# Kernel tuning notes

Measured on AMD Instinct MI355X. Metric: run time of the kernel, lower is better.

The kernel has to match this reference:

```python
import jax, jax.numpy as jnp
import numpy as np

B, D, H, E, TOPK = 65536, 1024, 512, 8, 2
LN_EPS = 1e-5
LB_WEIGHT = 0.01


def setup_inputs() -> dict:
    key = jax.random.key(0)
    ks = jax.random.split(key, 5)
    x = jax.random.normal(ks[0], (B, D), dtype=jnp.float32)
    W1 = jax.random.normal(ks[1], (D, H), dtype=jnp.float32) * 0.02
    b1 = jnp.zeros((H,), dtype=jnp.float32)
    ln_w = jnp.ones((H,), dtype=jnp.float32)
    ln_b = jnp.zeros((H,), dtype=jnp.float32)
    W2 = jax.random.normal(ks[2], (H, E), dtype=jnp.float32) * 0.02
    b2 = jnp.zeros((E,), dtype=jnp.float32)
    return {"x": x, "W1": W1, "b1": b1, "ln_w": ln_w, "ln_b": ln_b, "W2": W2, "b2": b2}


def _gate_logits(x, W1, b1, ln_w, ln_b, W2, b2):
    h = x @ W1 + b1                     # [B, H]
    mu = jnp.mean(h, axis=-1, keepdims=True)
    var = jnp.mean(jnp.square(h - mu), axis=-1, keepdims=True)
    h = (h - mu) * jax.lax.rsqrt(var + LN_EPS) * ln_w + ln_b
    h = jax.nn.gelu(h, approximate=False)  # torch nn.GELU default = exact erf
    return h @ W2 + b2                  # [B, E]


def reference(x, W1, b1, ln_w, ln_b, W2, b2):
    logits = _gate_logits(x, W1, b1, ln_w, ln_b, W2, b2)
    # sparse top-K routing (eval mode: no exploration noise)
    vals, idx = jax.lax.top_k(logits, TOPK)           # [B, K]
    rows = jnp.arange(logits.shape[0])[:, None]
    sparse = jnp.full_like(logits, -jnp.inf).at[rows, idx].set(vals)
    weights = jax.nn.softmax(sparse, axis=-1)         # zeros off top-k
    # Switch-style load-balance loss
    f = (weights > 0).astype(weights.dtype).mean(axis=0)  # fraction routed per expert
    P = weights.mean(axis=0)                              # mean gate prob per expert
    lb_loss = LB_WEIGHT * (E * jnp.sum(f * P))
    return weights, lb_loss
```

## Files before the change

### kernel.cpp

```cpp
#include <hip/hip_runtime.h>
#include <cstdint>
#include <cstddef>


typedef _Float16 f16;
typedef _Float16 f16x8 __attribute__((ext_vector_type(8)));
typedef float f32x4 __attribute__((ext_vector_type(4)));

#define B_ROWS 65536
#define D_DIM 1024
#define H_DIM 512
#define E_DIM 8
#define BM 64
#define BK 32
#define THREADS 256
#define NCHUNK 32
#define LDPX 40
#define SLABH 2560
#define BUFH 5120
#define IMG_CH (H_DIM * BK)
#define IMG_TOTAL (32 * IMG_CH)
#define GACC_OFF ((size_t)2 * IMG_TOTAL * sizeof(f16))

__global__ void prep_split(const float* __restrict__ W1,
                           f16* __restrict__ wh, f16* __restrict__ wl) {
  int id = blockIdx.x * 256 + threadIdx.x;
  int h = id & (H_DIM - 1);
  int kg = id >> 9;
  int c = kg >> 2;
  int kk0 = (kg & 3) * 8;
  int k0 = kg * 8;
  f16x8 hv, lv;
#pragma unroll
  for (int j = 0; j < 8; ++j) {
    float v = W1[(size_t)(k0 + j) * H_DIM + h] * 64.0f;
    f16 hi = (f16)v;
    hv[j] = hi;
    lv[j] = (f16)((v - (float)hi) * 256.0f);
  }
  size_t o = (size_t)c * IMG_CH + (size_t)h * BK + kk0;
  *(f16x8*)&wh[o] = hv;
  *(f16x8*)&wl[o] = lv;
}

__global__ void zero_acc(float* __restrict__ acc) {
  if (threadIdx.x < 16) acc[threadIdx.x] = 0.0f;
}

__global__ __launch_bounds__(THREADS, 2) void fused_main(
    const float* __restrict__ x,
    const f16* __restrict__ wh, const f16* __restrict__ wl,
    const float* __restrict__ b1, const float* __restrict__ lnw,
    const float* __restrict__ lnb, const float* __restrict__ W2,
    const float* __restrict__ b2, float* __restrict__ out,
    float* __restrict__ gacc) {
  __shared__ __align__(16) char pool[35584];
  f16* sx = (f16*)pool;

  const int tid = threadIdx.x;
  const int lane = tid & 63;
  const int wv = tid >> 6;
  const int l15 = lane & 15;
  const int l4 = lane >> 4;
  const int64_t row0 = (int64_t)blockIdx.x * BM;

  const int srow = tid >> 2;
  const int koff = (tid & 3) * 8;
  const int swo = srow * LDPX + koff;
  const float* xbase = x + (row0 + srow) * D_DIM + koff;

  const f16* whp = wh + (wv * 128 + l15) * BK + l4 * 8;

  f32x4 acc[4][8];
#pragma unroll
  for (int m = 0; m < 4; ++m)
#pragma unroll
    for (int n = 0; n < 8; ++n) acc[m][n] = (f32x4){0.f, 0.f, 0.f, 0.f};

  f16x8 setB[2][8];

#define ISSUE(si, C, half)                                                    \
  do {                                                                        \
    const f16* p = whp + (size_t)((C) & 31) * IMG_CH + (half) * 2048;         \
    setB[si][0] = *(const f16x8*)(p);                                         \
    setB[si][1] = *(const f16x8*)(p + 512);                                   \
    setB[si][2] = *(const f16x8*)(p + 1024);                                  \
    setB[si][3] = *(const f16x8*)(p + 1536);                                  \
    setB[si][4] = *(const f16x8*)(p + IMG_TOTAL);                             \
    setB[si][5] = *(const f16x8*)(p + IMG_TOTAL + 512);                       \
    setB[si][6] = *(const f16x8*)(p + IMG_TOTAL + 1024);                      \
    setB[si][7] = *(const f16x8*)(p + IMG_TOTAL + 1536);                      \
  } while (0)

#define CHM(MM, bufv)                                                         \
  do {                                                                        \
    const int ao = (bufv)*BUFH + ((MM)*16 + l15) * LDPX + l4 * 8;             \
    f16x8 ah = *(const f16x8*)&sx[ao];                                        \
    f16x8 al = *(const f16x8*)&sx[ao + SLABH];                                \
    f16x8 ahs;                                                                \
    _Pragma("unroll") for (int q = 0; q < 8; ++q) ahs[q] =                    \
        ah[q] * (f16)0.00390625f;                                             \
    _Pragma("unroll") for (int n = 0; n < 4; ++n)                             \
      acc[MM][n] = __builtin_amdgcn_mfma_f32_16x16x32_f16(                    \
          ah, setB[0][n], acc[MM][n], 0, 0, 0);                               \
    _Pragma("unroll") for (int n = 0; n < 4; ++n)                             \
      acc[MM][4 + n] = __builtin_amdgcn_mfma_f32_16x16x32_f16(                \
          ah, setB[1][n], acc[MM][4 + n], 0, 0, 0);                           \
    _Pragma("unroll") for (int n = 0; n < 4; ++n)                             \
      acc[MM][n] = __builtin_amdgcn_mfma_f32_16x16x32_f16(                    \
          al, setB[0][n], acc[MM][n], 0, 0, 0);                               \
    _Pragma("unroll") for (int n = 0; n < 4; ++n)                             \
      acc[MM][4 + n] = __builtin_amdgcn_mfma_f32_16x16x32_f16(                \
          al, setB[1][n], acc[MM][4 + n], 0, 0, 0);                           \
    _Pragma("unroll") for (int n = 0; n < 4; ++n)                             \
      acc[MM][n] = __builtin_amdgcn_mfma_f32_16x16x32_f16(                    \
          ahs, setB[0][4 + n], acc[MM][n], 0, 0, 0);                          \
    _Pragma("unroll") for (int n = 0; n < 4; ++n)                             \
      acc[MM][4 + n] = __builtin_amdgcn_mfma_f32_16x16x32_f16(                \
          ahs, setB[1][4 + n], acc[MM][4 + n], 0, 0, 0);                      \
  } while (0)

#define WRITE_SLAB(bufv)                                                      \
  do {                                                                        \
    float vv[8] = {xv0.x, xv0.y, xv0.z, xv0.w, xv1.x, xv1.y, xv1.z, xv1.w};   \
    f16x8 hv, lv;                                                             \
    _Pragma("unroll") for (int q = 0; q < 8; ++q) {                           \
      float t = vv[q] * 64.0f;                                                \
      f16 hh = (f16)t;                                                        \
      hv[q] = hh;                                                             \
      lv[q] = (f16)(t - (float)hh);                                           \
    }                                                                         \
    *(f16x8*)&sx[(bufv)*BUFH + swo] = hv;                                     \
    *(f16x8*)&sx[(bufv)*BUFH + SLABH + swo] = lv;                             \
  } while (0)

#define SLAB_BARRIER()                                                        \
  do {                                                                        \
    asm volatile("s_waitcnt lgkmcnt(0)" ::: "memory");                        \
    __builtin_amdgcn_s_barrier();                                             \
    __builtin_amdgcn_sched_barrier(0);                                        \
  } while (0)

  float4 xv0 = *(const float4*)(xbase);
  float4 xv1 = *(const float4*)(xbase + 4);
  WRITE_SLAB(0);
  ISSUE(0, 0, 0);
  ISSUE(1, 0, 1);
  xv0 = *(const float4*)(xbase + 32);
  xv1 = *(const float4*)(xbase + 36);
  SLAB_BARRIER();

  for (int c = 0; c < NCHUNK; ++c) {
    const int buf = c & 1;
    __builtin_amdgcn_s_setprio(1);
    CHM(0, buf);
    CHM(1, buf);
    CHM(2, buf);
    {
      const int ao = buf * BUFH + (3 * 16 + l15) * LDPX + l4 * 8;
      f16x8 ah = *(const f16x8*)&sx[ao];
      f16x8 al = *(const f16x8*)&sx[ao + SLABH];
      f16x8 ahs;
#pragma unroll
      for (int q = 0; q < 8; ++q) ahs[q] = ah[q] * (f16)0.00390625f;
#pragma unroll
      for (int n = 0; n < 4; ++n)
        acc[3][n] = __builtin_amdgcn_mfma_f32_16x16x32_f16(ah, setB[0][n], acc[3][n], 0, 0, 0);
#pragma unroll
      for (int n = 0; n < 4; ++n)
        acc[3][n] = __builtin_amdgcn_mfma_f32_16x16x32_f16(al, setB[0][n], acc[3][n], 0, 0, 0);
#pragma unroll
      for (int n = 0; n < 4; ++n)
        acc[3][n] = __builtin_amdgcn_mfma_f32_16x16x32_f16(ahs, setB[0][4 + n], acc[3][n], 0, 0, 0);
      __builtin_amdgcn_s_setprio(0);
      ISSUE(0, c + 1, 0);
      __builtin_amdgcn_s_setprio(1);
#pragma unroll
      for (int n = 0; n < 4; ++n)
        acc[3][4 + n] = __builtin_amdgcn_mfma_f32_16x16x32_f16(ah, setB[1][n], acc[3][4 + n], 0, 0, 0);
#pragma unroll
      for (int n = 0; n < 4; ++n)
        acc[3][4 + n] = __builtin_amdgcn_mfma_f32_16x16x32_f16(al, setB[1][n], acc[3][4 + n], 0, 0, 0);
#pragma unroll
      for (int n = 0; n < 4; ++n)
        acc[3][4 + n] = __builtin_amdgcn_mfma_f32_16x16x32_f16(ahs, setB[1][4 + n], acc[3][4 + n], 0, 0, 0);
      __builtin_amdgcn_s_setprio(0);
      ISSUE(1, c + 1, 1);
    }
    WRITE_SLAB(buf ^ 1);
    xv0 = *(const float4*)(xbase + ((c + 2) & 31) * 32);
    xv1 = *(const float4*)(xbase + ((c + 2) & 31) * 32 + 4);
    SLAB_BARRIER();
  }
#undef ISSUE
#undef CHM
#undef WRITE_SLAB
#undef SLAB_BARRIER
  __syncthreads();

  float* eW2T = (float*)pool;
  float* eStat = (float*)(pool + 24576);
  float* eLog = (float*)(pool + 26624);
  float* eMu = (float*)(pool + 34816);
  float* eRs = (float*)(pool + 35072);
  float* eFP = (float*)(pool + 35328);

  for (int i = tid; i < H_DIM; i += THREADS) {
    float4 wa = *(const float4*)&W2[i * 8];
    float4 wb = *(const float4*)&W2[i * 8 + 4];
    *(float4*)&eW2T[i * 12] = wa;
    *(float4*)&eW2T[i * 12 + 4] = wb;
  }
  if (tid < 16) eFP[tid] = 0.0f;

  float bb[8], lw[8], lb[8];
#pragma unroll
  for (int n = 0; n < 8; ++n) {
    int col = wv * 128 + n * 16 + l15;
    bb[n] = b1[col] * 4096.0f;
    lw[n] = lnw[col];
    lb[n] = lnb[col];
#pragma unroll
    for (int m = 0; m < 4; ++m)
#pragma unroll
      for (int r = 0; r < 4; ++r) acc[m][n][r] += bb[n];
  }

#pragma unroll
  for (int m = 0; m < 4; ++m) {
    float s1[4] = {0, 0, 0, 0};
    float s2[4] = {0, 0, 0, 0};
#pragma unroll
    for (int n = 0; n < 8; ++n)
#pragma unroll
      for (int r = 0; r < 4; ++r) {
        float vv = acc[m][n][r];
        s1[r] += vv;
        s2[r] = fmaf(vv, vv, s2[r]);
      }
#pragma unroll
    for (int d = 1; d < 16; d <<= 1)
#pragma unroll
      for (int r = 0; r < 4; ++r) {
        s1[r] += __shfl_xor(s1[r], d);
        s2[r] += __shfl_xor(s2[r], d);
      }
    if (l15 == 0) {
      int rb = m * 16 + l4 * 4;
#pragma unroll
      for (int r = 0; r < 4; ++r) {
        eStat[(wv * 64 + rb + r) * 2 + 0] = s1[r];
        eStat[(wv * 64 + rb + r) * 2 + 1] = s2[r];
      }
    }
  }
  __syncthreads();
  if (tid < BM) {
    float s1 = 0.0f, s2 = 0.0f;
#pragma unroll
    for (int w = 0; w < 4; ++w) {
      s1 += eStat[(w * 64 + tid) * 2 + 0];
      s2 += eStat[(w * 64 + tid) * 2 + 1];
    }
    float mu = s1 * (1.0f / 512.0f);
    float var = s2 * (1.0f / 512.0f) - mu * mu;
    eMu[tid] = mu;
    eRs[tid] = 1.0f / sqrtf(var + (1e-5f * 4096.0f * 4096.0f));
  }
  __syncthreads();

#pragma unroll
  for (int m = 0; m < 4; ++m) {
    int rb = m * 16 + l4 * 4;
#pragma unroll
    for (int r = 0; r < 4; ++r) {
      float mu_r = eMu[rb + r];
      float rs_r = eRs[rb + r];
      float lg[8];
#pragma unroll
      for (int e = 0; e < 8; ++e) lg[e] = 0.0f;
#pragma unroll
      for (int n = 0; n < 8; ++n) {
        int col = wv * 128 + n * 16 + l15;
        float hn = (acc[m][n][r] - mu_r) * rs_r;
        float y = fmaf(hn, lw[n], lb[n]);
        float g = 0.5f * y * (1.0f + erff(y * 0.70710678118654752440f));
        float4 w0 = *(const float4*)&eW2T[col * 12];
        float4 w1 = *(const float4*)&eW2T[col * 12 + 4];
        lg[0] = fmaf(g, w0.x, lg[0]);
        lg[1] = fmaf(g, w0.y, lg[1]);
        lg[2] = fmaf(g, w0.z, lg[2]);
        lg[3] = fmaf(g, w0.w, lg[3]);
        lg[4] = fmaf(g, w1.x, lg[4]);
        lg[5] = fmaf(g, w1.y, lg[5]);
        lg[6] = fmaf(g, w1.z, lg[6]);
        lg[7] = fmaf(g, w1.w, lg[7]);
      }
#pragma unroll
      for (int d = 1; d < 16; d <<= 1)
#pragma unroll
        for (int e = 0; e < 8; ++e) lg[e] += __shfl_xor(lg[e], d);
      if (l15 == 0) {
#pragma unroll
        for (int e = 0; e < 8; ++e) eLog[(wv * 64 + rb + r) * 8 + e] = lg[e];
      }
    }
  }
  __syncthreads();

  if (tid < BM) {
    float v[8];
#pragma unroll
    for (int e = 0; e < 8; ++e) {
      float s = b2[e];
#pragma unroll
      for (int w = 0; w < 4; ++w) s += eLog[(w * 64 + tid) * 8 + e];
      v[e] = s;
    }
    float m1 = v[0];
    int i1 = 0;
#pragma unroll
    for (int e = 1; e < 8; ++e)
      if (v[e] > m1) { m1 = v[e]; i1 = e; }
    float m2 = -3.0e38f;
    int i2 = -1;
#pragma unroll
    for (int e = 0; e < 8; ++e)
      if (e != i1 && v[e] > m2) { m2 = v[e]; i2 = e; }
    float dd = expf(m2 - m1);
    float inv = 1.0f / (1.0f + dd);
    float wA = inv, wB = dd * inv;
    float o[8];
#pragma unroll
    for (int e = 0; e < 8; ++e)
      o[e] = (e == i1) ? wA : ((e == i2) ? wB : 0.0f);
    float4* op = (float4*)&out[(row0 + tid) * 8];
    op[0] = (float4){o[0], o[1], o[2], o[3]};
    op[1] = (float4){o[4], o[5], o[6], o[7]};
    atomicAdd(&eFP[i1], 1.0f);
    atomicAdd(&eFP[i2], 1.0f);
    atomicAdd(&eFP[8 + i1], wA);
    atomicAdd(&eFP[8 + i2], wB);
  }
  __syncthreads();
  if (tid < 16) atomicAdd(&gacc[tid], eFP[tid]);
}

__global__ void lb_final(const float* __restrict__ gacc, float* __restrict__ out) {
  if (threadIdx.x == 0) {
    const float invB = 1.0f / 65536.0f;
    float s = 0.0f;
#pragma unroll
    for (int e = 0; e < 8; ++e) s += (gacc[e] * invB) * (gacc[8 + e] * invB);
    out[(size_t)B_ROWS * E_DIM] = 0.01f * 8.0f * s;
  }
}

extern "C" void kernel_launch(void* const* d_in, const int* in_sizes, int n_in,
                              void* d_out, int out_size, void* d_ws, size_t ws_size,
                              hipStream_t stream) {
  (void)in_sizes; (void)n_in; (void)out_size; (void)ws_size;
  const float* x = (const float*)d_in[0];
  const float* W1 = (const float*)d_in[1];
  const float* b1 = (const float*)d_in[2];
  const float* lnw = (const float*)d_in[3];
  const float* lnb = (const float*)d_in[4];
  const float* W2 = (const float*)d_in[5];
  const float* b2 = (const float*)d_in[6];
  float* out = (float*)d_out;
  f16* wh = (f16*)d_ws;
  f16* wl = wh + IMG_TOTAL;
  float* gacc = (float*)((char*)d_ws + GACC_OFF);

  zero_acc<<<1, 64, 0, stream>>>(gacc);
  prep_split<<<(D_DIM * H_DIM / 8) / 256, 256, 0, stream>>>(W1, wh, wl);
  fused_main<<<B_ROWS / BM, THREADS, 0, stream>>>(x, wh, wl, b1, lnw, lnb, W2, b2,
                                                  out, gacc);
  lb_final<<<1, 64, 0, stream>>>(gacc, out);
}
```

Baseline: 240.6 us.

## Double block row tile to 128 rows with 512 threads sharing W1 fragments

Each block now handles 128 rows with 8 waves arranged as 2 row groups × 4 column groups. Each W1 column slice is fetched by two waves, one per row group, so the same tile of W1 is applied to twice as many x rows and the per-row W1 load traffic is halved. In exchange the block uses more shared memory (about 46KB) and twice as many threads, which may reduce resident blocks per CU, and launch_bounds(…,2) with 512 threads may limit the registers available for the large accumulator array.

Result: slower. 251.5 us (+4.5%).

```diff
diff --git a/kernel.cpp b/kernel.cpp
--- a/kernel.cpp
+++ b/kernel.cpp
@@ -11,13 +11,13 @@
 #define D_DIM 1024
 #define H_DIM 512
 #define E_DIM 8
-#define BM 64
+#define BM 128
 #define BK 32
-#define THREADS 256
+#define THREADS 512
 #define NCHUNK 32
 #define LDPX 40
-#define SLABH 2560
-#define BUFH 5120
+#define SLABH 5120
+#define BUFH 10240
 #define IMG_CH (H_DIM * BK)
 #define IMG_TOTAL (32 * IMG_CH)
 #define GACC_OFF ((size_t)2 * IMG_TOTAL * sizeof(f16))
@@ -54,12 +54,14 @@
     const float* __restrict__ lnb, const float* __restrict__ W2,
     const float* __restrict__ b2, float* __restrict__ out,
     float* __restrict__ gacc) {
-  __shared__ __align__(16) char pool[35584];
+  __shared__ __align__(16) char pool[46208];
   f16* sx = (f16*)pool;
 
   const int tid = threadIdx.x;
   const int lane = tid & 63;
   const int wv = tid >> 6;
+  const int ng = wv & 3;
+  const int mg = wv >> 2;
   const int l15 = lane & 15;
   const int l4 = lane >> 4;
   const int64_t row0 = (int64_t)blockIdx.x * BM;
@@ -69,7 +71,7 @@
   const int swo = srow * LDPX + koff;
   const float* xbase = x + (row0 + srow) * D_DIM + koff;
 
-  const f16* whp = wh + (wv * 128 + l15) * BK + l4 * 8;
+  const f16* whp = wh + (ng * 128 + l15) * BK + l4 * 8;
 
   f32x4 acc[4][8];
 #pragma unroll
@@ -94,7 +96,7 @@
 
 #define CHM(MM, bufv)                                                         \
   do {                                                                        \
-    const int ao = (bufv)*BUFH + ((MM)*16 + l15) * LDPX + l4 * 8;             \
+    const int ao = (bufv)*BUFH + ((mg * 64 + (MM)*16 + l15)) * LDPX + l4 * 8; \
     f16x8 ah = *(const f16x8*)&sx[ao];                                        \
     f16x8 al = *(const f16x8*)&sx[ao + SLABH];                                \
     f16x8 ahs;                                                                \
@@ -157,7 +159,7 @@
     CHM(1, buf);
     CHM(2, buf);
     {
-      const int ao = buf * BUFH + (3 * 16 + l15) * LDPX + l4 * 8;
+      const int ao = buf * BUFH + (mg * 64 + 3 * 16 + l15) * LDPX + l4 * 8;
       f16x8 ah = *(const f16x8*)&sx[ao];
       f16x8 al = *(const f16x8*)&sx[ao + SLABH];
       f16x8 ahs;
@@ -200,23 +202,23 @@
 
   float* eW2T = (float*)pool;
   float* eStat = (float*)(pool + 24576);
-  float* eLog = (float*)(pool + 26624);
-  float* eMu = (float*)(pool + 34816);
-  float* eRs = (float*)(pool + 35072);
-  float* eFP = (float*)(pool + 35328);
-
-  for (int i = tid; i < H_DIM; i += THREADS) {
-    float4 wa = *(const float4*)&W2[i * 8];
-    float4 wb = *(const float4*)&W2[i * 8 + 4];
-    *(float4*)&eW2T[i * 12] = wa;
-    *(float4*)&eW2T[i * 12 + 4] = wb;
+  float* eLog = (float*)(pool + 28672);
+  float* eMu = (float*)(pool + 45056);
+  float* eRs = (float*)(pool + 45568);
+  float* eFP = (float*)(pool + 46080);
+
+  {
+    float4 wa = *(const float4*)&W2[tid * 8];
+    float4 wb = *(const float4*)&W2[tid * 8 + 4];
+    *(float4*)&eW2T[tid * 12] = wa;
+    *(float4*)&eW2T[tid * 12 + 4] = wb;
   }
   if (tid < 16) eFP[tid] = 0.0f;
 
   float bb[8], lw[8], lb[8];
 #pragma unroll
   for (int n = 0; n < 8; ++n) {
-    int col = wv * 128 + n * 16 + l15;
+    int col = ng * 128 + n * 16 + l15;
     bb[n] = b1[col] * 4096.0f;
     lw[n] = lnw[col];
     lb[n] = lnb[col];
@@ -246,11 +248,11 @@
         s2[r] += __shfl_xor(s2[r], d);
       }
     if (l15 == 0) {
-      int rb = m * 16 + l4 * 4;
+      int rb = mg * 64 + m * 16 + l4 * 4;
 #pragma unroll
       for (int r = 0; r < 4; ++r) {
-        eStat[(wv * 64 + rb + r) * 2 + 0] = s1[r];
-        eStat[(wv * 64 + rb + r) * 2 + 1] = s2[r];
+        eStat[(ng * 128 + rb + r) * 2 + 0] = s1[r];
+        eStat[(ng * 128 + rb + r) * 2 + 1] = s2[r];
       }
     }
   }
@@ -259,8 +261,8 @@
     float s1 = 0.0f, s2 = 0.0f;
 #pragma unroll
     for (int w = 0; w < 4; ++w) {
-      s1 += eStat[(w * 64 + tid) * 2 + 0];
-      s2 += eStat[(w * 64 + tid) * 2 + 1];
+      s1 += eStat[(w * 128 + tid) * 2 + 0];
+      s2 += eStat[(w * 128 + tid) * 2 + 1];
     }
     float mu = s1 * (1.0f / 512.0f);
     float var = s2 * (1.0f / 512.0f) - mu * mu;
@@ -271,7 +273,7 @@
 
 #pragma unroll
   for (int m = 0; m < 4; ++m) {
-    int rb = m * 16 + l4 * 4;
+    int rb = mg * 64 + m * 16 + l4 * 4;
 #pragma unroll
     for (int r = 0; r < 4; ++r) {
       float mu_r = eMu[rb + r];
@@ -281,7 +283,7 @@
       for (int e = 0; e < 8; ++e) lg[e] = 0.0f;
 #pragma unroll
       for (int n = 0; n < 8; ++n) {
-        int col = wv * 128 + n * 16 + l15;
+        int col = ng * 128 + n * 16 + l15;
         float hn = (acc[m][n][r] - mu_r) * rs_r;
         float y = fmaf(hn, lw[n], lb[n]);
         float g = 0.5f * y * (1.0f + erff(y * 0.70710678118654752440f));
@@ -302,7 +304,7 @@
         for (int e = 0; e < 8; ++e) lg[e] += __shfl_xor(lg[e], d);
       if (l15 == 0) {
 #pragma unroll
-        for (int e = 0; e < 8; ++e) eLog[(wv * 64 + rb + r) * 8 + e] = lg[e];
+        for (int e = 0; e < 8; ++e) eLog[(ng * 128 + rb + r) * 8 + e] = lg[e];
       }
     }
   }
@@ -314,7 +316,7 @@
     for (int e = 0; e < 8; ++e) {
       float s = b2[e];
 #pragma unroll
-      for (int w = 0; w < 4; ++w) s += eLog[(w * 64 + tid) * 8 + e];
+      for (int w = 0; w < 4; ++w) s += eLog[(w * 128 + tid) * 8 + e];
       v[e] = s;
     }
     float m1 = v[0];
```
